# Performance work log

Hardware: AMD Instinct MI355X
Metric: run time of the kernel (lower is better)

## Reference

```python
import jax, jax.numpy as jnp
import numpy as np

N_NODES = 50000
N_EDGES = 600000
F_IN = 128
HID = 128
N_CLASSES = 10


def _gcn_graph(edge_index, n_nodes):
    # PyG GCNConv: add self-loops, deg computed on target (col) with weight 1,
    # norm_e = deg^-1/2[src] * deg^-1/2[dst]
    src = jnp.concatenate([edge_index[0], jnp.arange(n_nodes, dtype=edge_index.dtype)])
    dst = jnp.concatenate([edge_index[1], jnp.arange(n_nodes, dtype=edge_index.dtype)])
    deg = jax.ops.segment_sum(jnp.ones_like(dst, dtype=jnp.float32), dst, num_segments=n_nodes)
    dinv = jnp.where(deg > 0, jax.lax.rsqrt(deg), 0.0)
    norm = dinv[src] * dinv[dst]  # [E+N]
    return src, dst, norm


def _gcn_layer(x, W, b, src, dst, norm, n_nodes):
    h = x @ W                      # [N, out] linear first (bias applied post-agg)
    m = h[src] * norm[:, None]     # gather + scale, [E+N, out]
    out = jax.ops.segment_sum(m, dst, num_segments=n_nodes)  # scatter-add
    return out + b


def setup_inputs() -> dict:
    key = jax.random.key(0)
    ks = jax.random.split(key, 4)
    x = jax.random.normal(ks[0], (N_NODES, F_IN), dtype=jnp.float32)
    edge_index = jax.random.randint(ks[1], (2, N_EDGES), 0, N_NODES, dtype=jnp.int64)
    # Glorot-ish init scale for weights
    W_stack = jax.random.normal(ks[2], (8, HID, HID), dtype=jnp.float32) * (1.0 / np.sqrt(HID))
    b_stack = jnp.zeros((8, HID), dtype=jnp.float32)
    W_out = jax.random.normal(ks[3], (HID, N_CLASSES), dtype=jnp.float32) * (1.0 / np.sqrt(HID))
    b_out = jnp.zeros((N_CLASSES,), dtype=jnp.float32)
    return {"x": x, "edge_index": edge_index, "W_stack": W_stack, "b_stack": b_stack,
            "W_out": W_out, "b_out": b_out}


def reference(x, edge_index, W_stack, b_stack, W_out, b_out):
    n_nodes = x.shape[0]
    src, dst, norm = _gcn_graph(edge_index, n_nodes)
    h = x
    for i in range(8):  # conv1..conv8 with ELU
        h = jax.nn.elu(_gcn_layer(h, W_stack[i], b_stack[i], src, dst, norm, n_nodes))
    # conv9: no activation
    return _gcn_layer(h, W_out, b_out, src, dst, norm, n_nodes)
```

## Files before the change

### kernel.cpp

```cpp
#include <hip/hip_runtime.h>
#include <math.h>

#define NN 50000
#define NE 600000
#define HID 128
#define NCLS 10
#define T2S 16

typedef __bf16 bf16x8 __attribute__((ext_vector_type(8)));
typedef float f32x16 __attribute__((ext_vector_type(16)));

__device__ __forceinline__ void split3(float f, ushort& h, ushort& m, ushort& l) {
    unsigned uh = __float_as_uint(f) & 0xffff0000u;
    float fm = f - __uint_as_float(uh);
    unsigned um = __float_as_uint(fm) & 0xffff0000u;
    float fl = fm - __uint_as_float(um);
    h = (ushort)(uh >> 16);
    m = (ushort)(um >> 16);
    l = (ushort)(__float_as_uint(fl) >> 16);
}


__global__ __launch_bounds__(256) void k_count(const int* __restrict__ edge,
                                               int* __restrict__ counts) {
    int e = blockIdx.x * 256 + threadIdx.x;
    if (e < NE) atomicAdd(&counts[edge[NE + e]], 1);
}

__device__ __forceinline__ int wave_incl_scan(int x, int lane) {
#pragma unroll
    for (int off = 1; off < 64; off <<= 1) {
        int y = __shfl_up(x, off, 64);
        if (lane >= off) x += y;
    }
    return x;
}

__global__ __launch_bounds__(256) void k_scan1(const int* __restrict__ counts,
                                               int* __restrict__ rowptr,
                                               int* __restrict__ bsum,
                                               float* __restrict__ dinv) {
    __shared__ int ws[4];
    int tid = threadIdx.x;
    int i = blockIdx.x * 256 + tid;
    int lane = tid & 63, wv = tid >> 6;
    int v = (i < NN) ? counts[i] : 0;
    if (i < NN) dinv[i] = rsqrtf((float)(v + 1));
    int x = wave_incl_scan(v, lane);
    if (lane == 63) ws[wv] = x;
    __syncthreads();
    int off = 0;
    for (int j = 0; j < wv; ++j) off += ws[j];
    if (i < NN) rowptr[i] = off + x - v;
    if (tid == 255) bsum[blockIdx.x] = off + x;
}

__global__ __launch_bounds__(256) void k_scan2(int* __restrict__ bsum, int n) {
    __shared__ int ws[4];
    int tid = threadIdx.x;
    int lane = tid & 63, wv = tid >> 6;
    int v = (tid < n) ? bsum[tid] : 0;
    int x = wave_incl_scan(v, lane);
    if (lane == 63) ws[wv] = x;
    __syncthreads();
    int off = 0;
    for (int j = 0; j < wv; ++j) off += ws[j];
    __syncthreads();
    if (tid < n) bsum[tid] = off + x - v;
}

__global__ __launch_bounds__(256) void k_scan3(int* __restrict__ rowptr,
                                               const int* __restrict__ bsum) {
    int i = blockIdx.x * 256 + threadIdx.x;
    if (i < NN) rowptr[i] += bsum[blockIdx.x];
    if (i == 0) rowptr[NN] = NE;
}

__global__ __launch_bounds__(256) void k_fill(const int* __restrict__ edge,
                                              const int* __restrict__ rowptr,
                                              int* __restrict__ cursor,
                                              const float* __restrict__ dinv,
                                              int2* __restrict__ csr) {
    int e = blockIdx.x * 256 + threadIdx.x;
    if (e >= NE) return;
    int s = edge[e], d = edge[NE + e];
    int slot = atomicSub(&cursor[d], 1) - 1;
    csr[rowptr[d] + slot] = make_int2(s, __float_as_int(dinv[s] * dinv[d]));
}


__global__ __launch_bounds__(256) void k_split_w(const float* __restrict__ Wst,
                                                 ushort* __restrict__ Wt4) {
    int i = blockIdx.x * 256 + threadIdx.x;
    if (i >= 8 * HID * HID) return;
    int l = i >> 14;
    int k = (i >> 7) & 127;
    int n = i & 127;
    ushort h, m, lo;
    split3(Wst[i], h, m, lo);
    int ks = k >> 4, r = k & 15;
    size_t base = ((((size_t)l * 3) * 8 + ks) * 128 + n) * 16 + r;
    const size_t pstride = (size_t)8 * 128 * 16;
    Wt4[base] = h;
    Wt4[base + pstride] = m;
    Wt4[base + 2 * pstride] = lo;
}


__global__ __launch_bounds__(256) void k_mfma_gemm(const float* __restrict__ H,
                                                   const ushort* __restrict__ Wt,
                                                   float* __restrict__ T) {
    __shared__ ushort As[3][128][40];
    int tid = threadIdx.x;
    int lane = tid & 63, w = tid >> 6;
    int wy = w >> 1, wx = w & 1;
    int l31 = lane & 31, lh = lane >> 5;
    int rowbase = blockIdx.x * 128;

    int arow = tid >> 1;
    int kh = (tid & 1) * 16;
    int garow = rowbase + arow;
    if (garow >= NN) garow = NN - 1;
    size_t aoff = (size_t)garow * HID;

    const ushort* wbase = Wt + ((size_t)wx * 64 + l31) * 16 + lh * 8;

    f32x16 acc[2][2] = {};

    for (int k0 = 0; k0 < HID; k0 += 32) {
        int ks0 = k0 >> 4;
        uint4 bf[2][3][2];
#pragma unroll
        for (int s = 0; s < 2; ++s)
#pragma unroll
            for (int p = 0; p < 3; ++p)
#pragma unroll
                for (int c = 0; c < 2; ++c)
                    bf[s][p][c] = *(const uint4*)(wbase +
                        (((size_t)p * 8 + ks0 + s) * 128 + c * 32) * 16);

        const float4* asrc = (const float4*)(H + aoff + k0 + kh);
        float4 af0 = asrc[0], af1 = asrc[1], af2 = asrc[2], af3 = asrc[3];
        float av[16] = {af0.x, af0.y, af0.z, af0.w, af1.x, af1.y, af1.z, af1.w,
                        af2.x, af2.y, af2.z, af2.w, af3.x, af3.y, af3.z, af3.w};
        union { ushort u[16]; uint4 v[2]; } ph, pm, pl;
#pragma unroll
        for (int q = 0; q < 16; ++q) split3(av[q], ph.u[q], pm.u[q], pl.u[q]);

        __syncthreads();
        *(uint4*)&As[0][arow][kh] = ph.v[0];
        *(uint4*)&As[0][arow][kh + 8] = ph.v[1];
        *(uint4*)&As[1][arow][kh] = pm.v[0];
        *(uint4*)&As[1][arow][kh + 8] = pm.v[1];
        *(uint4*)&As[2][arow][kh] = pl.v[0];
        *(uint4*)&As[2][arow][kh + 8] = pl.v[1];
        __syncthreads();

#pragma unroll
        for (int s = 0; s < 2; ++s) {
            int kk = s * 16 + lh * 8;
            bf16x8 a[3][2], b[3][2];
#pragma unroll
            for (int p = 0; p < 3; ++p) {
#pragma unroll
                for (int h = 0; h < 2; ++h)
                    a[p][h] = *(const bf16x8*)&As[p][wy * 64 + h * 32 + l31][kk];
#pragma unroll
                for (int c = 0; c < 2; ++c)
                    b[p][c] = *(const bf16x8*)&bf[s][p][c];
            }
#pragma unroll
            for (int h = 0; h < 2; ++h)
#pragma unroll
                for (int c = 0; c < 2; ++c)
                    acc[h][c] = __builtin_amdgcn_mfma_f32_32x32x16_bf16(a[0][h], b[0][c], acc[h][c], 0, 0, 0);
#pragma unroll
            for (int h = 0; h < 2; ++h)
#pragma unroll
                for (int c = 0; c < 2; ++c)
                    acc[h][c] = __builtin_amdgcn_mfma_f32_32x32x16_bf16(a[0][h], b[1][c], acc[h][c], 0, 0, 0);
#pragma unroll
            for (int h = 0; h < 2; ++h)
#pragma unroll
                for (int c = 0; c < 2; ++c)
                    acc[h][c] = __builtin_amdgcn_mfma_f32_32x32x16_bf16(a[1][h], b[0][c], acc[h][c], 0, 0, 0);
#pragma unroll
            for (int h = 0; h < 2; ++h)
#pragma unroll
                for (int c = 0; c < 2; ++c)
                    acc[h][c] = __builtin_amdgcn_mfma_f32_32x32x16_bf16(a[0][h], b[2][c], acc[h][c], 0, 0, 0);
#pragma unroll
            for (int h = 0; h < 2; ++h)
#pragma unroll
                for (int c = 0; c < 2; ++c)
                    acc[h][c] = __builtin_amdgcn_mfma_f32_32x32x16_bf16(a[1][h], b[1][c], acc[h][c], 0, 0, 0);
#pragma unroll
            for (int h = 0; h < 2; ++h)
#pragma unroll
                for (int c = 0; c < 2; ++c)
                    acc[h][c] = __builtin_amdgcn_mfma_f32_32x32x16_bf16(a[2][h], b[0][c], acc[h][c], 0, 0, 0);
        }
    }
#pragma unroll
    for (int h = 0; h < 2; ++h)
#pragma unroll
        for (int c = 0; c < 2; ++c)
#pragma unroll
            for (int reg = 0; reg < 16; ++reg) {
                int r = (reg & 3) + 8 * (reg >> 2) + 4 * lh;
                int gr = rowbase + wy * 64 + h * 32 + r;
                if (gr < NN)
                    T[(size_t)gr * HID + wx * 64 + c * 32 + l31] = acc[h][c][reg];
            }
}


__global__ __launch_bounds__(256) void k_gather_agg(const float* __restrict__ T,
                                                    float* __restrict__ Hout,
                                                    const int* __restrict__ rowptr,
                                                    const int2* __restrict__ csr,
                                                    const float* __restrict__ dinv,
                                                    const float* __restrict__ bias) {
    int lane = threadIdx.x & 63;
    int node = (blockIdx.x * 256 + threadIdx.x) >> 6;
    if (node >= NN) return;
    int slot = lane >> 5, l31 = lane & 31;

    int beg = rowptr[node], end = rowptr[node + 1];
    float sn = dinv[node];

    float4 acc = {0.f, 0.f, 0.f, 0.f};
    if (slot == 1) {
        float4 tv = ((const float4*)(T + (size_t)node * HID))[l31];
        float4 bv = ((const float4*)bias)[l31];
        float s2 = sn * sn;
        acc.x = s2 * tv.x + bv.x;
        acc.y = s2 * tv.y + bv.y;
        acc.z = s2 * tv.z + bv.z;
        acc.w = s2 * tv.w + bv.w;
    }

    const int2 zed = make_int2(0, 0);
    int p = beg + slot;
    int2 e0 = (p < end) ? csr[p] : zed;
    int2 e1 = (p + 2 < end) ? csr[p + 2] : zed;
    int2 e2 = (p + 4 < end) ? csr[p + 4] : zed;
    int2 e3 = (p + 6 < end) ? csr[p + 6] : zed;
    for (; p < end; p += 8) {
        float4 u0 = ((const float4*)(T + (size_t)e0.x * HID))[l31];
        float4 u1 = ((const float4*)(T + (size_t)e1.x * HID))[l31];
        float4 u2 = ((const float4*)(T + (size_t)e2.x * HID))[l31];
        float4 u3 = ((const float4*)(T + (size_t)e3.x * HID))[l31];
        float w0 = __int_as_float(e0.y), w1 = __int_as_float(e1.y);
        float w2 = __int_as_float(e2.y), w3 = __int_as_float(e3.y);
        e0 = (p + 8 < end) ? csr[p + 8] : zed;
        e1 = (p + 10 < end) ? csr[p + 10] : zed;
        e2 = (p + 12 < end) ? csr[p + 12] : zed;
        e3 = (p + 14 < end) ? csr[p + 14] : zed;
        acc.x += w0 * u0.x; acc.y += w0 * u0.y; acc.z += w0 * u0.z; acc.w += w0 * u0.w;
        acc.x += w1 * u1.x; acc.y += w1 * u1.y; acc.z += w1 * u1.z; acc.w += w1 * u1.w;
        acc.x += w2 * u2.x; acc.y += w2 * u2.y; acc.z += w2 * u2.z; acc.w += w2 * u2.w;
        acc.x += w3 * u3.x; acc.y += w3 * u3.y; acc.z += w3 * u3.z; acc.w += w3 * u3.w;
    }

    acc.x += __shfl_xor(acc.x, 32, 64);
    acc.y += __shfl_xor(acc.y, 32, 64);
    acc.z += __shfl_xor(acc.z, 32, 64);
    acc.w += __shfl_xor(acc.w, 32, 64);

    if (slot == 0) {
        float4 r = acc;
        r.x = r.x > 0.f ? r.x : expm1f(r.x);
        r.y = r.y > 0.f ? r.y : expm1f(r.y);
        r.z = r.z > 0.f ? r.z : expm1f(r.z);
        r.w = r.w > 0.f ? r.w : expm1f(r.w);
        ((float4*)(Hout + (size_t)node * HID))[l31] = r;
    }
}


__global__ __launch_bounds__(256) void k_matmul_out(const float* __restrict__ H,
                                                    const float* __restrict__ W,
                                                    float* __restrict__ T2) {
    __shared__ float Ws[128 * 11];
    int tid = threadIdx.x;
    for (int m = tid; m < HID * NCLS; m += 256) {
        int k = m / NCLS, c = m - k * NCLS;
        Ws[k * 11 + c] = W[m];
    }
    __syncthreads();
    int row = (blockIdx.x * 256 + tid) >> 4;
    int c16 = tid & 15;
    if (row >= NN) return;
    const float4* h4 = (const float4*)(H + (size_t)row * HID) + c16 * 2;
    float4 h0 = h4[0], h1 = h4[1];
    float hv[8] = {h0.x, h0.y, h0.z, h0.w, h1.x, h1.y, h1.z, h1.w};
    float acc[NCLS];
#pragma unroll
    for (int c = 0; c < NCLS; ++c) acc[c] = 0.f;
#pragma unroll
    for (int j = 0; j < 8; ++j) {
        const float* wr = &Ws[(c16 * 8 + j) * 11];
#pragma unroll
        for (int c = 0; c < NCLS; ++c) acc[c] += hv[j] * wr[c];
    }
#pragma unroll
    for (int off = 8; off >= 1; off >>= 1) {
#pragma unroll
        for (int c = 0; c < NCLS; ++c) acc[c] += __shfl_xor(acc[c], off, 16);
    }
    if (c16 < NCLS) T2[(size_t)row * T2S + c16] = acc[c16];
}

__global__ __launch_bounds__(256) void k_gather_out(const float* __restrict__ T2,
                                                    float* __restrict__ out,
                                                    const int* __restrict__ rowptr,
                                                    const int2* __restrict__ csr,
                                                    const float* __restrict__ dinv,
                                                    const float* __restrict__ bias) {
    int lane = threadIdx.x & 63;
    int node = (blockIdx.x * 256 + threadIdx.x) >> 6;
    if (node >= NN) return;
    int slot = lane >> 4, c = lane & 15;
    int beg = rowptr[node], end = rowptr[node + 1];
    float acc = 0.f;
    if (c < NCLS) {
        for (int i = beg + slot; i < end; i += 4) {
            int2 e = csr[i];
            acc += __int_as_float(e.y) * T2[(size_t)e.x * T2S + c];
        }
    }
    acc += __shfl_xor(acc, 16, 64);
    acc += __shfl_xor(acc, 32, 64);
    if (slot == 0 && c < NCLS) {
        float sn = dinv[node];
        sn *= sn;
        out[node * NCLS + c] = acc + sn * T2[(size_t)node * T2S + c] + bias[c];
    }
}


extern "C" void kernel_launch(void* const* d_in, const int* in_sizes, int n_in,
                              void* d_out, int out_size, void* d_ws, size_t ws_size,
                              hipStream_t stream) {
    (void)in_sizes; (void)n_in; (void)out_size; (void)ws_size;
    const float* x       = (const float*)d_in[0];
    const int*   edge    = (const int*)d_in[1];
    const float* W_stack = (const float*)d_in[2];
    const float* b_stack = (const float*)d_in[3];
    const float* W_out   = (const float*)d_in[4];
    const float* b_out   = (const float*)d_in[5];
    float* out = (float*)d_out;

    char* ws = (char*)d_ws;
    const size_t bigbuf = (size_t)NN * HID * sizeof(float);
    float* X      = (float*)ws;
    float* Y      = (float*)(ws + bigbuf);
    char*  p      = ws + 2 * bigbuf;
    int2*  csr    = (int2*)p;              p += sizeof(int2) * NE;
    float* dinv   = (float*)p;             p += sizeof(float) * NN;
    int*   rowptr = (int*)p;               p += sizeof(int) * (NN + 1);
    int*   counts = (int*)p;               p += sizeof(int) * NN;
    int*   bsum   = (int*)p;               p += sizeof(int) * 256;
    p = (char*)(((size_t)p + 15) & ~(size_t)15);
    ushort* Wt4 = (ushort*)p;  p += sizeof(ushort) * 8 * 3 * HID * HID;

    const int NB_N  = (NN + 255) / 256;
    const int NB_E  = (NE + 255) / 256;
    const int NB_G  = (NN + 127) / 128;
    const int NB_A  = (NN * 64 + 255) / 256;
    const int NB_W  = (NN * 64 + 255) / 256;
    const int NB_O  = (NN * 16 + 255) / 256;
    const int NB_SW = (8 * HID * HID + 255) / 256;

    hipMemsetAsync(counts, 0, sizeof(int) * NN, stream);
    k_count<<<NB_E, 256, 0, stream>>>(edge, counts);
    k_scan1<<<NB_N, 256, 0, stream>>>(counts, rowptr, bsum, dinv);
    k_scan2<<<1, 256, 0, stream>>>(bsum, NB_N);
    k_scan3<<<NB_N, 256, 0, stream>>>(rowptr, bsum);
    k_fill<<<NB_E, 256, 0, stream>>>(edge, rowptr, counts, dinv, csr);

    k_split_w<<<NB_SW, 256, 0, stream>>>(W_stack, Wt4);

    const float* Hin = x;
    for (int l = 0; l < 8; ++l) {
        k_mfma_gemm<<<NB_G, 256, 0, stream>>>(Hin, Wt4 + (size_t)l * 3 * HID * HID, Y);
        k_gather_agg<<<NB_A, 256, 0, stream>>>(Y, X, rowptr, csr, dinv,
                                               b_stack + (size_t)l * HID);
        Hin = X;
    }

    k_matmul_out<<<NB_O, 256, 0, stream>>>(X, W_out, Y);
    k_gather_out<<<NB_W, 256, 0, stream>>>(Y, out, rowptr, csr, dinv, b_out);
}
```

Baseline: 708.3 us.

## Load GEMM A fragments directly from global, drop shared-memory staging

Restructures the split-bf16 MFMA GEMM so each wave owns a 32-row by 128-column tile. Each lane reads its A row slice straight from global memory and splits it into three bf16 parts in registers, which removes the LDS staging buffer and both block barriers. The cost is that each lane now loads all W fragments (4 column tiles times 3 parts) per k-step, and the global A reads are strided per lane rather than cooperatively coalesced.

```diff
diff --git a/kernel.cpp b/kernel.cpp
--- a/kernel.cpp
+++ b/kernel.cpp
@@ -110,108 +110,64 @@
 __global__ __launch_bounds__(256) void k_mfma_gemm(const float* __restrict__ H,
                                                    const ushort* __restrict__ Wt,
                                                    float* __restrict__ T) {
-    __shared__ ushort As[3][128][40];
     int tid = threadIdx.x;
     int lane = tid & 63, w = tid >> 6;
-    int wy = w >> 1, wx = w & 1;
     int l31 = lane & 31, lh = lane >> 5;
     int rowbase = blockIdx.x * 128;
 
-    int arow = tid >> 1;
-    int kh = (tid & 1) * 16;
-    int garow = rowbase + arow;
-    if (garow >= NN) garow = NN - 1;
-    size_t aoff = (size_t)garow * HID;
-
-    const ushort* wbase = Wt + ((size_t)wx * 64 + l31) * 16 + lh * 8;
-
-    f32x16 acc[2][2] = {};
-
-    for (int k0 = 0; k0 < HID; k0 += 32) {
-        int ks0 = k0 >> 4;
-        uint4 bf[2][3][2];
-#pragma unroll
-        for (int s = 0; s < 2; ++s)
-#pragma unroll
-            for (int p = 0; p < 3; ++p)
-#pragma unroll
-                for (int c = 0; c < 2; ++c)
-                    bf[s][p][c] = *(const uint4*)(wbase +
-                        (((size_t)p * 8 + ks0 + s) * 128 + c * 32) * 16);
-
-        const float4* asrc = (const float4*)(H + aoff + k0 + kh);
-        float4 af0 = asrc[0], af1 = asrc[1], af2 = asrc[2], af3 = asrc[3];
-        float av[16] = {af0.x, af0.y, af0.z, af0.w, af1.x, af1.y, af1.z, af1.w,
-                        af2.x, af2.y, af2.z, af2.w, af3.x, af3.y, af3.z, af3.w};
-        union { ushort u[16]; uint4 v[2]; } ph, pm, pl;
-#pragma unroll
-        for (int q = 0; q < 16; ++q) split3(av[q], ph.u[q], pm.u[q], pl.u[q]);
-
-        __syncthreads();
-        *(uint4*)&As[0][arow][kh] = ph.v[0];
-        *(uint4*)&As[0][arow][kh + 8] = ph.v[1];
-        *(uint4*)&As[1][arow][kh] = pm.v[0];
-        *(uint4*)&As[1][arow][kh + 8] = pm.v[1];
-        *(uint4*)&As[2][arow][kh] = pl.v[0];
-        *(uint4*)&As[2][arow][kh + 8] = pl.v[1];
-        __syncthreads();
-
-#pragma unroll
-        for (int s = 0; s < 2; ++s) {
-            int kk = s * 16 + lh * 8;
-            bf16x8 a[3][2], b[3][2];
-#pragma unroll
-            for (int p = 0; p < 3; ++p) {
-#pragma unroll
-                for (int h = 0; h < 2; ++h)
-                    a[p][h] = *(const bf16x8*)&As[p][wy * 64 + h * 32 + l31][kk];
-#pragma unroll
-                for (int c = 0; c < 2; ++c)
-                    b[p][c] = *(const bf16x8*)&bf[s][p][c];
-            }
-#pragma unroll
-            for (int h = 0; h < 2; ++h)
-#pragma unroll
-                for (int c = 0; c < 2; ++c)
-                    acc[h][c] = __builtin_amdgcn_mfma_f32_32x32x16_bf16(a[0][h], b[0][c], acc[h][c], 0, 0, 0);
-#pragma unroll
-            for (int h = 0; h < 2; ++h)
-#pragma unroll
-                for (int c = 0; c < 2; ++c)
-                    acc[h][c] = __builtin_amdgcn_mfma_f32_32x32x16_bf16(a[0][h], b[1][c], acc[h][c], 0, 0, 0);
-#pragma unroll
-            for (int h = 0; h < 2; ++h)
-#pragma unroll
-                for (int c = 0; c < 2; ++c)
-                    acc[h][c] = __builtin_amdgcn_mfma_f32_32x32x16_bf16(a[1][h], b[0][c], acc[h][c], 0, 0, 0);
-#pragma unroll
-            for (int h = 0; h < 2; ++h)
-#pragma unroll
-                for (int c = 0; c < 2; ++c)
-                    acc[h][c] = __builtin_amdgcn_mfma_f32_32x32x16_bf16(a[0][h], b[2][c], acc[h][c], 0, 0, 0);
-#pragma unroll
-            for (int h = 0; h < 2; ++h)
-#pragma unroll
-                for (int c = 0; c < 2; ++c)
-                    acc[h][c] = __builtin_amdgcn_mfma_f32_32x32x16_bf16(a[1][h], b[1][c], acc[h][c], 0, 0, 0);
-#pragma unroll
-            for (int h = 0; h < 2; ++h)
-#pragma unroll
-                for (int c = 0; c < 2; ++c)
-                    acc[h][c] = __builtin_amdgcn_mfma_f32_32x32x16_bf16(a[2][h], b[0][c], acc[h][c], 0, 0, 0);
+    int grow = rowbase + w * 32 + l31;
+    if (grow >= NN) grow = NN - 1;
+    const float* arow = H + (size_t)grow * HID + lh * 8;
+
+    const ushort* wbase = Wt + (size_t)l31 * 16 + lh * 8;
+
+    f32x16 acc[4] = {};
+
+#pragma unroll 2
+    for (int s = 0; s < 8; ++s) {
+        const float4* ap = (const float4*)(arow + s * 16);
+        float4 f0 = ap[0], f1 = ap[1];
+        float av[8] = {f0.x, f0.y, f0.z, f0.w, f1.x, f1.y, f1.z, f1.w};
+        union { ushort u[8]; bf16x8 v; } ah, am, al;
+#pragma unroll
+        for (int q = 0; q < 8; ++q) split3(av[q], ah.u[q], am.u[q], al.u[q]);
+
+        uint4 bf[3][4];
+#pragma unroll
+        for (int p = 0; p < 3; ++p)
+#pragma unroll
+            for (int c = 0; c < 4; ++c)
+                bf[p][c] = *(const uint4*)(wbase + (((size_t)p * 8 + s) * 128 + c * 32) * 16);
+
+#pragma unroll
+        for (int c = 0; c < 4; ++c)
+            acc[c] = __builtin_amdgcn_mfma_f32_32x32x16_bf16(ah.v, *(const bf16x8*)&bf[0][c], acc[c], 0, 0, 0);
+#pragma unroll
+        for (int c = 0; c < 4; ++c)
+            acc[c] = __builtin_amdgcn_mfma_f32_32x32x16_bf16(ah.v, *(const bf16x8*)&bf[1][c], acc[c], 0, 0, 0);
+#pragma unroll
+        for (int c = 0; c < 4; ++c)
+            acc[c] = __builtin_amdgcn_mfma_f32_32x32x16_bf16(am.v, *(const bf16x8*)&bf[0][c], acc[c], 0, 0, 0);
+#pragma unroll
+        for (int c = 0; c < 4; ++c)
+            acc[c] = __builtin_amdgcn_mfma_f32_32x32x16_bf16(ah.v, *(const bf16x8*)&bf[2][c], acc[c], 0, 0, 0);
+#pragma unroll
+        for (int c = 0; c < 4; ++c)
+            acc[c] = __builtin_amdgcn_mfma_f32_32x32x16_bf16(am.v, *(const bf16x8*)&bf[1][c], acc[c], 0, 0, 0);
+#pragma unroll
+        for (int c = 0; c < 4; ++c)
+            acc[c] = __builtin_amdgcn_mfma_f32_32x32x16_bf16(al.v, *(const bf16x8*)&bf[0][c], acc[c], 0, 0, 0);
+    }
+
+#pragma unroll
+    for (int c = 0; c < 4; ++c)
+#pragma unroll
+        for (int reg = 0; reg < 16; ++reg) {
+            int r = (reg & 3) + 8 * (reg >> 2) + 4 * lh;
+            int gr = rowbase + w * 32 + r;
+            if (gr < NN)
+                T[(size_t)gr * HID + c * 32 + l31] = acc[c][reg];
         }
-    }
-#pragma unroll
-    for (int h = 0; h < 2; ++h)
-#pragma unroll
-        for (int c = 0; c < 2; ++c)
-#pragma unroll
-            for (int reg = 0; reg < 16; ++reg) {
-                int r = (reg & 3) + 8 * (reg >> 2) + 4 * lh;
-                int gr = rowbase + wy * 64 + h * 32 + r;
-                if (gr < NN)
-                    T[(size_t)gr * HID + wx * 64 + c * 32 + l31] = acc[h][c][reg];
-            }
 }
 
 
```

Measured after the change: 724.6 us. +2.3%, slower.
